# Performance work log

Measured on AMD Instinct MI355X. Metric: run time of the kernel, lower is better.

The kernel has to match this reference:

```python
import jax, jax.numpy as jnp
import numpy as np

N, K, F_IN, F_OUT, P = 50000, 32, 64, 64, 3


def setup_inputs() -> dict:
    key = jax.random.key(0)
    k1, k2, k3, k4, k5 = jax.random.split(key, 5)
    h = jax.random.normal(k1, (N, F_IN), dtype=jnp.float32)
    pos = jax.random.normal(k2, (N, P), dtype=jnp.float32)
    neighbor_idx = jax.random.randint(k3, (N, K), 0, N, dtype=jnp.int32)
    weight = jax.random.normal(k4, (K * F_IN, F_OUT), dtype=jnp.float32) * 0.02
    bias_p = jax.random.normal(k5, (1, F_OUT), dtype=jnp.float32) * 0.02
    return {"h": h, "pos": pos, "neighbor_idx": neighbor_idx,
            "weight": weight, "bias_p": bias_p}


def reference(h, pos, neighbor_idx, weight, bias_p):
    n, k = neighbor_idx.shape
    msgs = h[neighbor_idx]                      # [N, K, F_IN] gather
    diff = pos[:, None, :] - pos[neighbor_idx]  # [N, K, P]
    sq = jnp.sum(diff * diff, axis=2, keepdims=True)  # [N, K, 1]
    # torch: dist[dist==0] = 0.5 ; safe-sqrt avoids NaN grads at 0
    dist = jnp.where(sq == 0.0, 0.5, jnp.sqrt(jnp.where(sq == 0.0, 1.0, sq)))
    wow = (msgs / dist).reshape(n, k * h.shape[1])  # [N, K*F_IN]
    h1 = wow @ weight + bias_p                   # [N, F_OUT]
    return jax.nn.leaky_relu(h1, negative_slope=0.01)
```

## Files before the change

kernel.cpp:

```cpp
#include <hip/hip_runtime.h>


#define N_NODES 50000
#define KN      32
#define FIN     64
#define FOUT    64
#define MTILE   32
#define EPITCH  35

typedef __attribute__((ext_vector_type(4))) float    f32x4;
typedef __attribute__((ext_vector_type(8))) _Float16 f16x8;

static __device__ __forceinline__ f16x8 dec8i(unsigned int x, unsigned int y) {
    union { unsigned int w[4]; f16x8 v; } r;
    unsigned int xh = x >> 16, yh = y >> 16;
    r.w[0] = 0x64006400u | ((x  & 0xFFu) << 2) | ((x  & 0xFF00u) << 10);
    r.w[1] = 0x64006400u | ((xh & 0xFFu) << 2) | ((xh & 0xFF00u) << 10);
    r.w[2] = 0x64006400u | ((y  & 0xFFu) << 2) | ((y  & 0xFF00u) << 10);
    r.w[3] = 0x64006400u | ((yh & 0xFFu) << 2) | ((yh & 0xFF00u) << 10);
    return r.v;
}

__global__ void k_prep(const float* __restrict__ w, _Float16* __restrict__ wf,
                       const float* __restrict__ h, unsigned char* __restrict__ hq,
                       const float* __restrict__ pos, float4* __restrict__ posx) {
    __shared__ float s_w[64 * 64];
    const int tid = threadIdx.x;
    if (blockIdx.x < 32) {
        const int kn = blockIdx.x;
        for (int p = tid; p < 64 * 64; p += 256)
            s_w[p] = w[kn * 64 * 64 + p];
        __syncthreads();
        const int t = tid >> 6, lane = tid & 63;
        const int lm = lane & 15, q = lane >> 4;
        #pragma unroll
        for (int jh = 0; jh < 2; ++jh) {
            f16x8 o;
            #pragma unroll
            for (int i = 0; i < 8; ++i)
                o[i] = (_Float16)s_w[(q * 16 + jh * 8 + i) * 64 + t * 16 + lm];
            *(f16x8*)(wf + ((kn * 2 + jh) * 4 + t) * 512 + lane * 8) = o;
        }
    } else {
        const int r   = (blockIdx.x - 32) * 64 + (tid >> 2);
        const int sub = tid & 3;
        if (r < N_NODES) {
            const float* hr = h + (size_t)r * FIN + sub * 16;
            float v[16];
            float amax = 0.f;
            #pragma unroll
            for (int i = 0; i < 4; ++i) {
                float4 t4 = ((const float4*)hr)[i];
                v[i * 4 + 0] = t4.x; v[i * 4 + 1] = t4.y;
                v[i * 4 + 2] = t4.z; v[i * 4 + 3] = t4.w;
                amax = fmaxf(amax, fmaxf(fmaxf(fabsf(t4.x), fabsf(t4.y)),
                                         fmaxf(fabsf(t4.z), fabsf(t4.w))));
            }
            amax = fmaxf(amax, __shfl_xor(amax, 1));
            amax = fmaxf(amax, __shfl_xor(amax, 2));
            float scale = fmaxf(amax, 1e-30f) * (1.0f / 126.0f);
            float inv   = 126.0f / fmaxf(amax, 1e-30f);
            union { unsigned char c[16]; uint4 u4; } o;
            #pragma unroll
            for (int i = 0; i < 16; ++i) {
                int q8 = __float2int_rn(v[i] * inv);
                o.c[i] = (unsigned char)(q8 + 128);
            }
            *(uint4*)(hq + (size_t)r * 64 + sub * 16) = o.u4;
            if (sub == 0) {
                float4 px;
                px.x = pos[r * 3 + 0]; px.y = pos[r * 3 + 1]; px.z = pos[r * 3 + 2];
                px.w = scale;
                posx[r] = px;
            }
        }
    }
}

__global__ __launch_bounds__(256, 4) void k_main(
        const unsigned char* __restrict__ hq,
        const float4*        __restrict__ posx,
        const int*           __restrict__ nidx,
        const _Float16*      __restrict__ wf,
        const float*         __restrict__ bias,
        float*               __restrict__ out)
{
    __shared__ __align__(16) char smem[2 * 32 * 68 * 4];
    int2*  s_e   = (int2*)smem;
    float* s_red = (float*)smem;

    const int tid = threadIdx.x;
    const int m0  = blockIdx.x * MTILE;
    const int lane = tid & 63, kg = tid >> 6;
    const int lm = lane & 15, q = lane >> 4;

    for (int it = 0; it < 4; ++it) {
        int pp = it * 64 + lane;
        int m  = pp >> 3;
        int kn = kg * 8 + (pp & 7);
        int node = m0 + m;
        int idx = 0; float c1 = 0.f;
        if (node < N_NODES) {
            idx = nidx[node * KN + kn];
            float4 pn = posx[node];
            float4 pi = posx[idx];
            float dx = pn.x - pi.x, dy = pn.y - pi.y, dz = pn.z - pi.z;
            float sq = dx * dx + dy * dy + dz * dz;
            float scl = (sq == 0.f) ? 2.0f : rsqrtf(sq);
            c1 = pi.w * scl * 0.25f;
        }
        s_e[m * EPITCH + kn] = make_int2(idx, __float_as_int(c1));
    }

    const _Float16* pb = wf + lane * 8;

    f32x4 acc[2][4] = {};

    #pragma unroll 1
    for (int j = 0; j < 8; ++j) {
        const int kn = kg * 8 + j;
        int2 e0 = s_e[(lm     ) * EPITCH + kn];
        int2 e1 = s_e[(lm + 16) * EPITCH + kn];
        uint4 d0 = *(const uint4*)(hq + (size_t)e0.x * 64 + q * 16);
        uint4 d1 = *(const uint4*)(hq + (size_t)e1.x * 64 + q * 16);
        const _Float16 c0 = (_Float16)__int_as_float(e0.y);
        const _Float16 c1 = (_Float16)__int_as_float(e1.y);
        const _Float16 K = (_Float16)1536.0f;

        {
            const _Float16* pbb = pb + (kn * 2 + 0) * 2048;
            f16x8 b0 = *(const f16x8*)(pbb);
            f16x8 b1 = *(const f16x8*)(pbb + 512);
            f16x8 b2 = *(const f16x8*)(pbb + 1024);
            f16x8 b3 = *(const f16x8*)(pbb + 1536);
            f16x8 a0 = (dec8i(d0.x, d0.y) - K) * c0;
            f16x8 a1 = (dec8i(d1.x, d1.y) - K) * c1;
            acc[0][0] = __builtin_amdgcn_mfma_f32_16x16x32_f16(a0, b0, acc[0][0], 0, 0, 0);
            acc[0][1] = __builtin_amdgcn_mfma_f32_16x16x32_f16(a0, b1, acc[0][1], 0, 0, 0);
            acc[0][2] = __builtin_amdgcn_mfma_f32_16x16x32_f16(a0, b2, acc[0][2], 0, 0, 0);
            acc[0][3] = __builtin_amdgcn_mfma_f32_16x16x32_f16(a0, b3, acc[0][3], 0, 0, 0);
            acc[1][0] = __builtin_amdgcn_mfma_f32_16x16x32_f16(a1, b0, acc[1][0], 0, 0, 0);
            acc[1][1] = __builtin_amdgcn_mfma_f32_16x16x32_f16(a1, b1, acc[1][1], 0, 0, 0);
            acc[1][2] = __builtin_amdgcn_mfma_f32_16x16x32_f16(a1, b2, acc[1][2], 0, 0, 0);
            acc[1][3] = __builtin_amdgcn_mfma_f32_16x16x32_f16(a1, b3, acc[1][3], 0, 0, 0);
        }
        {
            const _Float16* pbb = pb + (kn * 2 + 1) * 2048;
            f16x8 b0 = *(const f16x8*)(pbb);
            f16x8 b1 = *(const f16x8*)(pbb + 512);
            f16x8 b2 = *(const f16x8*)(pbb + 1024);
            f16x8 b3 = *(const f16x8*)(pbb + 1536);
            f16x8 a0 = (dec8i(d0.z, d0.w) - K) * c0;
            f16x8 a1 = (dec8i(d1.z, d1.w) - K) * c1;
            acc[0][0] = __builtin_amdgcn_mfma_f32_16x16x32_f16(a0, b0, acc[0][0], 0, 0, 0);
            acc[0][1] = __builtin_amdgcn_mfma_f32_16x16x32_f16(a0, b1, acc[0][1], 0, 0, 0);
            acc[0][2] = __builtin_amdgcn_mfma_f32_16x16x32_f16(a0, b2, acc[0][2], 0, 0, 0);
            acc[0][3] = __builtin_amdgcn_mfma_f32_16x16x32_f16(a0, b3, acc[0][3], 0, 0, 0);
            acc[1][0] = __builtin_amdgcn_mfma_f32_16x16x32_f16(a1, b0, acc[1][0], 0, 0, 0);
            acc[1][1] = __builtin_amdgcn_mfma_f32_16x16x32_f16(a1, b1, acc[1][1], 0, 0, 0);
            acc[1][2] = __builtin_amdgcn_mfma_f32_16x16x32_f16(a1, b2, acc[1][2], 0, 0, 0);
            acc[1][3] = __builtin_amdgcn_mfma_f32_16x16x32_f16(a1, b3, acc[1][3], 0, 0, 0);
        }
    }

    __syncthreads();

    float* reg = s_red + (kg & 1) * (32 * 68);
    if (kg < 2) {
        #pragma unroll
        for (int mt = 0; mt < 2; ++mt)
            #pragma unroll
            for (int t = 0; t < 4; ++t)
                #pragma unroll
                for (int r = 0; r < 4; ++r)
                    reg[(mt * 16 + q * 4 + r) * 68 + t * 16 + lm] = acc[mt][t][r];
    }
    __syncthreads();
    if (kg >= 2) {
        #pragma unroll
        for (int mt = 0; mt < 2; ++mt)
            #pragma unroll
            for (int t = 0; t < 4; ++t)
                #pragma unroll
                for (int r = 0; r < 4; ++r)
                    reg[(mt * 16 + q * 4 + r) * 68 + t * 16 + lm] += acc[mt][t][r];
    }
    __syncthreads();

    const int row = tid >> 3, c0e = (tid & 7) * 8;
    const int node = m0 + row;
    if (node < N_NODES) {
        #pragma unroll
        for (int i = 0; i < 2; ++i) {
            int c = c0e + i * 4;
            f32x4 v0 = *(const f32x4*)(s_red + row * 68 + c);
            f32x4 v1 = *(const f32x4*)(s_red + 32 * 68 + row * 68 + c);
            f32x4 bb = *(const f32x4*)(bias + c);
            f32x4 o = v0 + v1 + bb;
            #pragma unroll
            for (int jj = 0; jj < 4; ++jj) o[jj] = o[jj] > 0.f ? o[jj] : 0.01f * o[jj];
            *(f32x4*)(out + node * FOUT + c) = o;
        }
    }
}

extern "C" void kernel_launch(void* const* d_in, const int* in_sizes, int n_in,
                              void* d_out, int out_size, void* d_ws, size_t ws_size,
                              hipStream_t stream) {
    const float* h    = (const float*)d_in[0];
    const float* pos  = (const float*)d_in[1];
    const int*   nidx = (const int*)d_in[2];
    const float* w    = (const float*)d_in[3];
    const float* bias = (const float*)d_in[4];
    float* out = (float*)d_out;

    _Float16*      wf   = (_Float16*)d_ws;
    unsigned char* hq   = (unsigned char*)d_ws + 262144;
    float4*        posx = (float4*)((char*)d_ws + 262144 + 3200000);

    const int h_blocks = (N_NODES + 63) / 64;
    k_prep<<<32 + h_blocks, 256, 0, stream>>>(w, wf, h, hq, pos, posx);
    k_main<<<(N_NODES + MTILE - 1) / MTILE, 256, 0, stream>>>(hq, posx, nidx, wf, bias, out);
}
```

Before: 116.0 us.

## Switch main GEMM to int8 MFMA with per-column weight scales and 64-row tiles

Weights are now quantized to int8 with per-output-column scales, replacing fp16, and the activation int8 codes are fed straight into int8 16x16x64 MFMA instead of being decoded to fp16. Each MFMA result is dequantized in fp32 using the per-edge activation scale and the per-column weight scale. The node tile grows from 32 to 64 rows so each weight fragment is reused across more rows, and launch bounds drop to 3 blocks per CU. The cost is many scalar FMAs per MFMA for dequantization, more registers and shared memory, and lower occupancy. Accuracy is also at risk from quantizing the weights.

```diff
diff --git a/kernel.cpp b/kernel.cpp
--- a/kernel.cpp
+++ b/kernel.cpp
@@ -5,42 +5,43 @@
 #define KN      32
 #define FIN     64
 #define FOUT    64
-#define MTILE   32
+#define MTILE   64
 #define EPITCH  35
 
-typedef __attribute__((ext_vector_type(4))) float    f32x4;
-typedef __attribute__((ext_vector_type(8))) _Float16 f16x8;
-
-static __device__ __forceinline__ f16x8 dec8i(unsigned int x, unsigned int y) {
-    union { unsigned int w[4]; f16x8 v; } r;
-    unsigned int xh = x >> 16, yh = y >> 16;
-    r.w[0] = 0x64006400u | ((x  & 0xFFu) << 2) | ((x  & 0xFF00u) << 10);
-    r.w[1] = 0x64006400u | ((xh & 0xFFu) << 2) | ((xh & 0xFF00u) << 10);
-    r.w[2] = 0x64006400u | ((y  & 0xFFu) << 2) | ((y  & 0xFF00u) << 10);
-    r.w[3] = 0x64006400u | ((yh & 0xFFu) << 2) | ((yh & 0xFF00u) << 10);
-    return r.v;
-}
-
-__global__ void k_prep(const float* __restrict__ w, _Float16* __restrict__ wf,
-                       const float* __restrict__ h, unsigned char* __restrict__ hq,
+typedef __attribute__((ext_vector_type(4))) float f32x4;
+typedef __attribute__((ext_vector_type(4))) int   i32x4;
+
+__global__ void k_prep(const float* __restrict__ w, char* __restrict__ wq,
+                       float* __restrict__ wsc,
+                       const float* __restrict__ h, char* __restrict__ hq,
                        const float* __restrict__ pos, float4* __restrict__ posx) {
     __shared__ float s_w[64 * 64];
+    __shared__ float s_scale[64];
     const int tid = threadIdx.x;
     if (blockIdx.x < 32) {
         const int kn = blockIdx.x;
         for (int p = tid; p < 64 * 64; p += 256)
             s_w[p] = w[kn * 64 * 64 + p];
         __syncthreads();
+        if (tid < 64) {
+            float amax = 0.f;
+            for (int r = 0; r < 64; ++r)
+                amax = fmaxf(amax, fabsf(s_w[r * 64 + tid]));
+            float s = fmaxf(amax, 1e-30f) * (1.0f / 126.0f);
+            s_scale[tid] = 126.0f / fmaxf(amax, 1e-30f);
+            wsc[kn * 64 + tid] = s;
+        }
+        __syncthreads();
         const int t = tid >> 6, lane = tid & 63;
-        const int lm = lane & 15, q = lane >> 4;
-        #pragma unroll
-        for (int jh = 0; jh < 2; ++jh) {
-            f16x8 o;
-            #pragma unroll
-            for (int i = 0; i < 8; ++i)
-                o[i] = (_Float16)s_w[(q * 16 + jh * 8 + i) * 64 + t * 16 + lm];
-            *(f16x8*)(wf + ((kn * 2 + jh) * 4 + t) * 512 + lane * 8) = o;
-        }
+        const int lm = lane & 15, qq = lane >> 4;
+        const float inv = s_scale[t * 16 + lm];
+        union { char c[16]; uint4 u4; } o;
+        #pragma unroll
+        for (int i = 0; i < 16; ++i) {
+            float wv = s_w[(qq * 16 + i) * 64 + t * 16 + lm];
+            o.c[i] = (char)__float2int_rn(wv * inv);
+        }
+        *(uint4*)(wq + (size_t)((kn * 4 + t) * 64 + lane) * 16) = o.u4;
     } else {
         const int r   = (blockIdx.x - 32) * 64 + (tid >> 2);
         const int sub = tid & 3;
@@ -60,12 +61,10 @@
             amax = fmaxf(amax, __shfl_xor(amax, 2));
             float scale = fmaxf(amax, 1e-30f) * (1.0f / 126.0f);
             float inv   = 126.0f / fmaxf(amax, 1e-30f);
-            union { unsigned char c[16]; uint4 u4; } o;
-            #pragma unroll
-            for (int i = 0; i < 16; ++i) {
-                int q8 = __float2int_rn(v[i] * inv);
-                o.c[i] = (unsigned char)(q8 + 128);
-            }
+            union { char c[16]; uint4 u4; } o;
+            #pragma unroll
+            for (int i = 0; i < 16; ++i)
+                o.c[i] = (char)__float2int_rn(v[i] * inv);
             *(uint4*)(hq + (size_t)r * 64 + sub * 16) = o.u4;
             if (sub == 0) {
                 float4 px;
@@ -77,15 +76,16 @@
     }
 }
 
-__global__ __launch_bounds__(256, 4) void k_main(
-        const unsigned char* __restrict__ hq,
-        const float4*        __restrict__ posx,
-        const int*           __restrict__ nidx,
-        const _Float16*      __restrict__ wf,
-        const float*         __restrict__ bias,
-        float*               __restrict__ out)
+__global__ __launch_bounds__(256, 3) void k_main(
+        const char*   __restrict__ hq,
+        const float4* __restrict__ posx,
+        const int*    __restrict__ nidx,
+        const char*   __restrict__ wq,
+        const float*  __restrict__ wsc,
+        const float*  __restrict__ bias,
+        float*        __restrict__ out)
 {
-    __shared__ __align__(16) char smem[2 * 32 * 68 * 4];
+    __shared__ __align__(16) char smem[2 * 64 * 68 * 4];
     int2*  s_e   = (int2*)smem;
     float* s_red = (float*)smem;
 
@@ -94,7 +94,7 @@
     const int lane = tid & 63, kg = tid >> 6;
     const int lm = lane & 15, q = lane >> 4;
 
-    for (int it = 0; it < 4; ++it) {
+    for (int it = 0; it < 8; ++it) {
         int pp = it * 64 + lane;
         int m  = pp >> 3;
         int kn = kg * 8 + (pp & 7);
@@ -107,68 +107,59 @@
             float dx = pn.x - pi.x, dy = pn.y - pi.y, dz = pn.z - pi.z;
             float sq = dx * dx + dy * dy + dz * dz;
             float scl = (sq == 0.f) ? 2.0f : rsqrtf(sq);
-            c1 = pi.w * scl * 0.25f;
+            c1 = pi.w * scl;
         }
         s_e[m * EPITCH + kn] = make_int2(idx, __float_as_int(c1));
     }
 
-    const _Float16* pb = wf + lane * 8;
-
-    f32x4 acc[2][4] = {};
+    f32x4 acc[4][4] = {};
+    const i32x4 zero = {0, 0, 0, 0};
 
     #pragma unroll 1
     for (int j = 0; j < 8; ++j) {
         const int kn = kg * 8 + j;
         int2 e0 = s_e[(lm     ) * EPITCH + kn];
         int2 e1 = s_e[(lm + 16) * EPITCH + kn];
-        uint4 d0 = *(const uint4*)(hq + (size_t)e0.x * 64 + q * 16);
-        uint4 d1 = *(const uint4*)(hq + (size_t)e1.x * 64 + q * 16);
-        const _Float16 c0 = (_Float16)__int_as_float(e0.y);
-        const _Float16 c1 = (_Float16)__int_as_float(e1.y);
-        const _Float16 K = (_Float16)1536.0f;
-
-        {
-            const _Float16* pbb = pb + (kn * 2 + 0) * 2048;
-            f16x8 b0 = *(const f16x8*)(pbb);
-            f16x8 b1 = *(const f16x8*)(pbb + 512);
-            f16x8 b2 = *(const f16x8*)(pbb + 1024);
-            f16x8 b3 = *(const f16x8*)(pbb + 1536);
-            f16x8 a0 = (dec8i(d0.x, d0.y) - K) * c0;
-            f16x8 a1 = (dec8i(d1.x, d1.y) - K) * c1;
-            acc[0][0] = __builtin_amdgcn_mfma_f32_16x16x32_f16(a0, b0, acc[0][0], 0, 0, 0);
-            acc[0][1] = __builtin_amdgcn_mfma_f32_16x16x32_f16(a0, b1, acc[0][1], 0, 0, 0);
-            acc[0][2] = __builtin_amdgcn_mfma_f32_16x16x32_f16(a0, b2, acc[0][2], 0, 0, 0);
-            acc[0][3] = __builtin_amdgcn_mfma_f32_16x16x32_f16(a0, b3, acc[0][3], 0, 0, 0);
-            acc[1][0] = __builtin_amdgcn_mfma_f32_16x16x32_f16(a1, b0, acc[1][0], 0, 0, 0);
-            acc[1][1] = __builtin_amdgcn_mfma_f32_16x16x32_f16(a1, b1, acc[1][1], 0, 0, 0);
-            acc[1][2] = __builtin_amdgcn_mfma_f32_16x16x32_f16(a1, b2, acc[1][2], 0, 0, 0);
-            acc[1][3] = __builtin_amdgcn_mfma_f32_16x16x32_f16(a1, b3, acc[1][3], 0, 0, 0);
-        }
-        {
-            const _Float16* pbb = pb + (kn * 2 + 1) * 2048;
-            f16x8 b0 = *(const f16x8*)(pbb);
-            f16x8 b1 = *(const f16x8*)(pbb + 512);
-            f16x8 b2 = *(const f16x8*)(pbb + 1024);
-            f16x8 b3 = *(const f16x8*)(pbb + 1536);
-            f16x8 a0 = (dec8i(d0.z, d0.w) - K) * c0;
-            f16x8 a1 = (dec8i(d1.z, d1.w) - K) * c1;
-            acc[0][0] = __builtin_amdgcn_mfma_f32_16x16x32_f16(a0, b0, acc[0][0], 0, 0, 0);
-            acc[0][1] = __builtin_amdgcn_mfma_f32_16x16x32_f16(a0, b1, acc[0][1], 0, 0, 0);
-            acc[0][2] = __builtin_amdgcn_mfma_f32_16x16x32_f16(a0, b2, acc[0][2], 0, 0, 0);
-            acc[0][3] = __builtin_amdgcn_mfma_f32_16x16x32_f16(a0, b3, acc[0][3], 0, 0, 0);
-            acc[1][0] = __builtin_amdgcn_mfma_f32_16x16x32_f16(a1, b0, acc[1][0], 0, 0, 0);
-            acc[1][1] = __builtin_amdgcn_mfma_f32_16x16x32_f16(a1, b1, acc[1][1], 0, 0, 0);
-            acc[1][2] = __builtin_amdgcn_mfma_f32_16x16x32_f16(a1, b2, acc[1][2], 0, 0, 0);
-            acc[1][3] = __builtin_amdgcn_mfma_f32_16x16x32_f16(a1, b3, acc[1][3], 0, 0, 0);
+        int2 e2 = s_e[(lm + 32) * EPITCH + kn];
+        int2 e3 = s_e[(lm + 48) * EPITCH + kn];
+        i32x4 a0 = *(const i32x4*)(hq + (size_t)e0.x * 64 + q * 16);
+        i32x4 a1 = *(const i32x4*)(hq + (size_t)e1.x * 64 + q * 16);
+        i32x4 a2 = *(const i32x4*)(hq + (size_t)e2.x * 64 + q * 16);
+        i32x4 a3 = *(const i32x4*)(hq + (size_t)e3.x * 64 + q * 16);
+        const char* pq = wq + (size_t)(kn * 4) * 1024 + lane * 16;
+        i32x4 b0 = *(const i32x4*)(pq);
+        i32x4 b1 = *(const i32x4*)(pq + 1024);
+        i32x4 b2 = *(const i32x4*)(pq + 2048);
+        i32x4 b3 = *(const i32x4*)(pq + 3072);
+        const float* wsk = wsc + kn * 64;
+        float sb[4] = { wsk[lm], wsk[16 + lm], wsk[32 + lm], wsk[48 + lm] };
+        float sa[4][4];
+        #pragma unroll
+        for (int mt = 0; mt < 4; ++mt)
+            #pragma unroll
+            for (int r = 0; r < 4; ++r)
+                sa[mt][r] = __int_as_float(s_e[(mt * 16 + q * 4 + r) * EPITCH + kn].y);
+
+        #pragma unroll
+        for (int mt = 0; mt < 4; ++mt) {
+            i32x4 a = (mt == 0) ? a0 : (mt == 1) ? a1 : (mt == 2) ? a2 : a3;
+            #pragma unroll
+            for (int t = 0; t < 4; ++t) {
+                i32x4 b = (t == 0) ? b0 : (t == 1) ? b1 : (t == 2) ? b2 : b3;
+                i32x4 D = __builtin_amdgcn_mfma_i32_16x16x64_i8(a, b, zero, 0, 0, 0);
+                #pragma unroll
+                for (int r = 0; r < 4; ++r)
+                    acc[mt][t][r] += sa[mt][r] * sb[t] * (float)D[r];
+            }
         }
     }
 
     __syncthreads();
 
-    float* reg = s_red + (kg & 1) * (32 * 68);
+    float* reg = s_red + (kg & 1) * (64 * 68);
     if (kg < 2) {
         #pragma unroll
-        for (int mt = 0; mt < 2; ++mt)
+        for (int mt = 0; mt < 4; ++mt)
             #pragma unroll
             for (int t = 0; t < 4; ++t)
                 #pragma unroll
@@ -178,7 +169,7 @@
     __syncthreads();
     if (kg >= 2) {
         #pragma unroll
-        for (int mt = 0; mt < 2; ++mt)
+        for (int mt = 0; mt < 4; ++mt)
             #pragma unroll
             for (int t = 0; t < 4; ++t)
                 #pragma unroll
@@ -187,14 +178,14 @@
     }
     __syncthreads();
 
-    const int row = tid >> 3, c0e = (tid & 7) * 8;
+    const int row = tid >> 2, c0e = (tid & 3) * 16;
     const int node = m0 + row;
     if (node < N_NODES) {
         #pragma unroll
-        for (int i = 0; i < 2; ++i) {
+        for (int i = 0; i < 4; ++i) {
             int c = c0e + i * 4;
             f32x4 v0 = *(const f32x4*)(s_red + row * 68 + c);
-            f32x4 v1 = *(const f32x4*)(s_red + 32 * 68 + row * 68 + c);
+            f32x4 v1 = *(const f32x4*)(s_red + 64 * 68 + row * 68 + c);
             f32x4 bb = *(const f32x4*)(bias + c);
             f32x4 o = v0 + v1 + bb;
             #pragma unroll
@@ -214,11 +205,12 @@
     const float* bias = (const float*)d_in[4];
     float* out = (float*)d_out;
 
-    _Float16*      wf   = (_Float16*)d_ws;
-    unsigned char* hq   = (unsigned char*)d_ws + 262144;
-    float4*        posx = (float4*)((char*)d_ws + 262144 + 3200000);
+    char*   wq   = (char*)d_ws;
+    float*  wsc  = (float*)((char*)d_ws + 131072);
+    char*   hq   = (char*)d_ws + 262144;
+    float4* posx = (float4*)((char*)d_ws + 262144 + 3200000);
 
     const int h_blocks = (N_NODES + 63) / 64;
-    k_prep<<<32 + h_blocks, 256, 0, stream>>>(w, wf, h, hq, pos, posx);
-    k_main<<<(N_NODES + MTILE - 1) / MTILE, 256, 0, stream>>>(hq, posx, nidx, wf, bias, out);
+    k_prep<<<32 + h_blocks, 256, 0, stream>>>(w, wq, wsc, h, hq, pos, posx);
+    k_main<<<(N_NODES + MTILE - 1) / MTILE, 256, 0, stream>>>(hq, posx, nidx, wq, wsc, bias, out);
 }
```

Result: slower. 128.2 us (+10.5%).
